# Performance work log

Measured on AMD Instinct MI355X. Metric: run time of the kernel, lower is better.

## Reference

```python
import jax, jax.numpy as jnp
import numpy as np

EPS = 1e-6
FRAME_SEQLEN = 1560          # hardcoded in source kv-cache path
LOCAL_ATTN_SIZE = 4
MAX_ATTN = LOCAL_ATTN_SIZE * FRAME_SEQLEN  # 6240
NUM_HEADS = 12


def _ln(x, w=None, b=None):
    mu = jnp.mean(x, axis=-1, keepdims=True)
    var = jnp.mean(jnp.square(x - mu), axis=-1, keepdims=True)
    y = (x - mu) * jax.lax.rsqrt(var + EPS)
    return y * w + b if w is not None else y


def _rms(x, w):
    return x * jax.lax.rsqrt(jnp.mean(jnp.square(x), axis=-1, keepdims=True) + EPS) * w


def _rope_tables(freqs_real, freqs_imag, nf, hh, ww, start_frame, c):
    # split freqs columns into temporal / height / width parts, as in causal_rope_apply
    s0 = c - 2 * (c // 3)
    s1 = c // 3
    def build(tab):
        f0 = tab[start_frame:start_frame + nf, :s0]       # [nf, s0]
        f1 = tab[:hh, s0:s0 + s1]                          # [hh, s1]
        f2 = tab[:ww, s0 + s1:]                            # [ww, s1]
        return jnp.concatenate([
            jnp.broadcast_to(f0[:, None, None, :], (nf, hh, ww, s0)),
            jnp.broadcast_to(f1[None, :, None, :], (nf, hh, ww, s1)),
            jnp.broadcast_to(f2[None, None, :, :], (nf, hh, ww, s1)),
        ], axis=-1).reshape(nf * hh * ww, 1, c)
    return build(freqs_real), build(freqs_imag)


def _causal_rope(x, cos, sin):
    # x: [B, L, n, d] with interleaved (real, imag) pairs; cos/sin: [1, L, 1, c]
    B, L, n, d = x.shape
    c = d // 2
    xr = x.reshape(B, L, n, c, 2)
    a, b = xr[..., 0], xr[..., 1]
    out = jnp.stack([a * cos - b * sin, a * sin + b * cos], axis=-1)
    return out.reshape(B, L, n, d)


def _sdpa(q, k, v):
    scale = q.shape[-1] ** -0.5
    s = jnp.einsum('bqhd,bkhd->bhqk', q, k) * scale
    a = jax.nn.softmax(s, axis=-1)
    return jnp.einsum('bhqk,bkhd->bqhd', a, v)


def _forward(hidden_states, encoder_hidden_states, temb, freqs_real, freqs_imag,
             k_cache, v_cache, scale_shift_table,
             Wq, bq, Wk, bk, Wv, bv, Wo, bo, norm_q_w, norm_k_w,
             saln_w, saln_b,
             cWq, cbq, cWk, cbk, cWv, cbv, cWo, cbo, c_norm_q_w, c_norm_k_w,
             W1, b1, W2, b2,
             current_start, grid_h, grid_w):
    B, L, D = hidden_states.shape
    nf = temb.shape[1]
    fs = L // nf                     # == FRAME_SEQLEN
    H = NUM_HEADS
    hd = D // H
    c = hd // 2
    x = hidden_states.astype(jnp.float32)

    # AdaLN modulation per frame
    e = scale_shift_table + temb                     # [B, nf, 6, D]
    shift, scale, gate = e[:, :, 0:1], e[:, :, 1:2], e[:, :, 2:3]
    c_shift, c_scale, c_gate = e[:, :, 3:4], e[:, :, 4:5], e[:, :, 5:6]

    nh = (_ln(x).reshape(B, nf, fs, D) * (1 + scale) + shift).reshape(B, L, D)

    # self-attn projections + rms_norm_across_heads qk norm
    q = _rms(nh @ Wq.T + bq, norm_q_w).reshape(B, L, H, hd)
    k = _rms(nh @ Wk.T + bk, norm_k_w).reshape(B, L, H, hd)
    v = (nh @ Wv.T + bv).reshape(B, L, H, hd)

    # causal RoPE with temporal offset current_start // 1560
    start_frame = current_start // FRAME_SEQLEN
    cos, sin = _rope_tables(freqs_real, freqs_imag, nf, grid_h, grid_w, start_frame, c)
    cos, sin = cos[None], sin[None]                  # [1, L, 1, c]
    rq = _causal_rope(q, cos, sin)
    rk = _causal_rope(k, cos, sin)

    # kv-cache update (no-eviction branch: num_new + local_end_prev == cache size)
    kc = jax.lax.stop_gradient(k_cache).at[:, current_start:current_start + L].set(rk)
    vc = jax.lax.stop_gradient(v_cache).at[:, current_start:current_start + L].set(v)
    local_end = current_start + L
    win_lo = max(0, local_end - MAX_ATTN)
    attn = _sdpa(rq, kc[:, win_lo:local_end], vc[:, win_lo:local_end]).reshape(B, L, D)
    attn = attn @ Wo.T + bo

    # gated residual + affine LN (self_attn_residual_norm)
    x = x + (attn.reshape(B, nf, fs, D) * gate).reshape(B, L, D)
    n2 = _ln(x, saln_w, saln_b)

    # T2V cross attention
    ctx = encoder_hidden_states.astype(jnp.float32)
    Lc = ctx.shape[1]
    cq = _rms(n2 @ cWq.T + cbq, c_norm_q_w).reshape(B, L, H, hd)
    ck = _rms(ctx @ cWk.T + cbk, c_norm_k_w).reshape(B, Lc, H, hd)
    cv = (ctx @ cWv.T + cbv).reshape(B, Lc, H, hd)
    ca = _sdpa(cq, ck, cv).reshape(B, L, D) @ cWo.T + cbo

    # residual + LN with c_scale/c_shift modulation (cross_attn_residual_norm)
    x = x + ca
    n3 = (_ln(x).reshape(B, nf, fs, D) * (1 + c_scale) + c_shift).reshape(B, L, D)

    # FFN (gelu tanh) + gated residual (MulAdd)
    ff = jax.nn.gelu(n3 @ W1.T + b1, approximate=True) @ W2.T + b2
    x = x + (ff.reshape(B, nf, fs, D) * c_gate).reshape(B, L, D)
    return x


def setup_inputs() -> dict:
    key = jax.random.key(0)
    D, FF, H = 1536, 8960, NUM_HEADS
    NF, FS = 2, FRAME_SEQLEN
    L = NF * FS
    CACHE = MAX_ATTN
    CTX = 512
    hd = D // H
    c = hd // 2
    ks = iter(jax.random.split(key, 40))
    def nrm(shape, s=1.0):
        return jax.random.normal(next(ks), shape, jnp.float32) * s

    def part(dim):
        inv = 1.0 / (10000.0 ** (np.arange(0, dim, 2, dtype=np.float64) / dim))
        f = np.outer(np.arange(1024, dtype=np.float64), inv)
        return np.cos(f), np.sin(f)
    c0, s0 = part(2 * (c - 2 * (c // 3)))
    c1, s1 = part(2 * (c // 3))
    c2, s2 = part(2 * (c // 3))
    freqs_real = jnp.asarray(np.concatenate([c0, c1, c2], axis=1), jnp.float32)  # [1024, 64]
    freqs_imag = jnp.asarray(np.concatenate([s0, s1, s2], axis=1), jnp.float32)

    return dict(
        hidden_states=nrm((1, L, D)),
        encoder_hidden_states=nrm((1, CTX, D)),
        temb=nrm((1, NF, 6, D), 0.5),
        freqs_real=freqs_real, freqs_imag=freqs_imag,
        k_cache=nrm((1, CACHE, H, hd), 0.5),
        v_cache=nrm((1, CACHE, H, hd), 0.5),
        scale_shift_table=nrm((1, 6, D), D ** -0.5),
        Wq=nrm((D, D), 0.02), bq=jnp.zeros((D,), jnp.float32),
        Wk=nrm((D, D), 0.02), bk=jnp.zeros((D,), jnp.float32),
        Wv=nrm((D, D), 0.02), bv=jnp.zeros((D,), jnp.float32),
        Wo=nrm((D, D), 0.02), bo=jnp.zeros((D,), jnp.float32),
        norm_q_w=jnp.ones((D,), jnp.float32), norm_k_w=jnp.ones((D,), jnp.float32),
        saln_w=jnp.ones((D,), jnp.float32), saln_b=jnp.zeros((D,), jnp.float32),
        cWq=nrm((D, D), 0.02), cbq=jnp.zeros((D,), jnp.float32),
        cWk=nrm((D, D), 0.02), cbk=jnp.zeros((D,), jnp.float32),
        cWv=nrm((D, D), 0.02), cbv=jnp.zeros((D,), jnp.float32),
        cWo=nrm((D, D), 0.02), cbo=jnp.zeros((D,), jnp.float32),
        c_norm_q_w=jnp.ones((D,), jnp.float32), c_norm_k_w=jnp.ones((D,), jnp.float32),
        W1=nrm((FF, D), 0.02), b1=jnp.zeros((FF,), jnp.float32),
        W2=nrm((D, FF), 0.02), b2=jnp.zeros((D,), jnp.float32),
        current_start=2 * FS, grid_h=30, grid_w=52,
    )


def reference(hidden_states, encoder_hidden_states, temb, freqs_real, freqs_imag,
              k_cache, v_cache, scale_shift_table,
              Wq, bq, Wk, bk, Wv, bv, Wo, bo, norm_q_w, norm_k_w,
              saln_w, saln_b,
              cWq, cbq, cWk, cbk, cWv, cbv, cWo, cbo, c_norm_q_w, c_norm_k_w,
              W1, b1, W2, b2,
              current_start, grid_h, grid_w):
    return _forward(hidden_states, encoder_hidden_states, temb, freqs_real, freqs_imag,
                    k_cache, v_cache, scale_shift_table,
                    Wq, bq, Wk, bk, Wv, bv, Wo, bo, norm_q_w, norm_k_w,
                    saln_w, saln_b,
                    cWq, cbq, cWk, cbk, cWv, cbv, cWo, cbo, c_norm_q_w, c_norm_k_w,
                    W1, b1, W2, b2,
                    current_start, grid_h, grid_w)
```

## Files before the change

### kernel.cpp

```cpp
#include <hip/hip_runtime.h>
#include <hip/hip_bf16.h>
#include <stdint.h>

typedef uint16_t u16;
typedef uint32_t u32;
typedef float    f32x4  __attribute__((ext_vector_type(4)));
typedef __bf16   bf16x8 __attribute__((ext_vector_type(8)));
typedef u16      u16x8  __attribute__((ext_vector_type(8)));
typedef u16      u16x4  __attribute__((ext_vector_type(4)));
typedef float    f32x4v __attribute__((ext_vector_type(4)));


__device__ __forceinline__ u16 f2bf(float f) {
    u32 u = __builtin_bit_cast(u32, f);
    u32 r = u + 0x7fffu + ((u >> 16) & 1u);
    return (u16)(r >> 16);
}
__device__ __forceinline__ float bfbits2f(u32 ubits) {
    return __builtin_bit_cast(float, ubits << 16);
}
__device__ __forceinline__ u32 cvtpk(float a, float b) {
    u32 r;
    asm("v_cvt_pk_bf16_f32 %0, %1, %2" : "=v"(r) : "v"(a), "v"(b));
    return r;
}
__device__ __forceinline__ bf16x8 loadb8(const u16* p) {
    u16x8 u = *(const u16x8*)p;
    return __builtin_bit_cast(bf16x8, u);
}
__device__ __forceinline__ f32x4 mfma16(bf16x8 a, bf16x8 b, f32x4 c) {
    return __builtin_amdgcn_mfma_f32_16x16x32_bf16(a, b, c, 0, 0, 0);
}
__device__ __forceinline__ void gload16(const u16* gp, u16* lp) {
    __builtin_amdgcn_global_load_lds((const __attribute__((address_space(1))) void*)gp,
                                     (__attribute__((address_space(3))) void*)lp, 16, 0, 0);
}
__device__ __forceinline__ float blockSum(float v, volatile float* buf, int t) {
#pragma unroll
    for (int o = 1; o < 64; o <<= 1) v += __shfl_xor(v, o);
    if ((t & 63) == 0) buf[t >> 6] = v;
    __syncthreads();
    float r = buf[0] + buf[1] + buf[2] + buf[3];
    __syncthreads();
    return r;
}

struct ConvJob { const float* s; u16* d; int n4; };
struct ConvJobs { ConvJob j[12]; int cnt; };

__global__ void k_conv(ConvJobs js) {
    int tid = blockIdx.x * blockDim.x + threadIdx.x;
    int stride = gridDim.x * blockDim.x;
    for (int q = 0; q < js.cnt; q++) {
        const f32x4v* s = (const f32x4v*)js.j[q].s;
        u16x4* d = (u16x4*)js.j[q].d;
        int n4 = js.j[q].n4;
        for (int i = tid; i < n4; i += stride) {
            f32x4v v = s[i];
            u16x4 o;
            o[0] = f2bf(v[0]); o[1] = f2bf(v[1]); o[2] = f2bf(v[2]); o[3] = f2bf(v[3]);
            d[i] = o;
        }
    }
}

__global__ void k_mod(const float* __restrict__ sst, const float* __restrict__ temb, float* __restrict__ e) {
    int i = blockIdx.x * 256 + threadIdx.x;
    if (i < 18432) e[i] = sst[i % 9216] + temb[i];
}

__global__ void k_cachecvt(const float* __restrict__ kc, const float* __restrict__ vc,
                           u16* __restrict__ Ka, u16* __restrict__ Va) {
    int b = blockIdx.x;
    int hd = (b % 6) * 256 + threadIdx.x;
    int p0 = (b / 6) * 4;
    int h = hd >> 7, d = hd & 127;
    u16x4 vv;
#pragma unroll
    for (int j = 0; j < 4; j++) {
        long src = (long)(p0 + j) * 1536 + hd;
        Ka[(long)h * 798720 + (long)(p0 + j) * 128 + d] = f2bf(kc[src]);
        vv[j] = f2bf(vc[src]);
    }
    *(u16x4*)&Va[(long)h * 798720 + (long)d * 6240 + p0] = vv;
}

__global__ __launch_bounds__(256) void k_ln(const float* __restrict__ x, u16* __restrict__ out,
                                            const float* __restrict__ mulp, const float* __restrict__ addp,
                                            int perFrame, int plusOne) {
    __shared__ float buf[4];
    const int row = blockIdx.x, t = threadIdx.x;
    const float* xr = x + (long)row * 1536;
    float v[6];
    float s = 0.f;
#pragma unroll
    for (int k = 0; k < 6; k++) { v[k] = xr[t + k * 256]; s += v[k]; }
    s = blockSum(s, buf, t);
    float mu = s * (1.f / 1536.f);
    float q = 0.f;
#pragma unroll
    for (int k = 0; k < 6; k++) { float d = v[k] - mu; q += d * d; }
    q = blockSum(q, buf, t);
    float inv = rsqrtf(q * (1.f / 1536.f) + 1e-6f);
    const int fo = perFrame ? (row / 1560) * 9216 : 0;
    u16* orow = out + (long)row * 1536;
    float add1 = plusOne ? 1.f : 0.f;
#pragma unroll
    for (int k = 0; k < 6; k++) {
        int c = t + k * 256;
        float m = mulp[fo + c] + add1;
        float y = (v[k] - mu) * inv * m + addp[fo + c];
        orow[c] = f2bf(y);
    }
}

__global__ __launch_bounds__(256) void k_rmsrope(const u16* __restrict__ in, int ld, int colOff,
                                                 const float* __restrict__ bias,
                                                 const float* __restrict__ w,
                                                 u16* __restrict__ out, long headStride,
                                                 const float* __restrict__ fr, const float* __restrict__ fi,
                                                 int doRope) {
    __shared__ float buf[4];
    const int row = blockIdx.x, t = threadIdx.x;
    const u32* xr = (const u32*)(in + (long)row * ld + colOff);
    const float2* b2 = (const float2*)bias;
    float px[3], py[3];
    float ss = 0.f;
#pragma unroll
    for (int i = 0; i < 3; i++) {
        u32 u = xr[t * 3 + i];
        float2 bb = b2[t * 3 + i];
        px[i] = bfbits2f(u & 0xffffu) + bb.x;
        py[i] = bfbits2f(u >> 16) + bb.y;
        ss += px[i] * px[i] + py[i] * py[i];
    }
    ss = blockSum(ss, buf, t);
    float inv = rsqrtf(ss * (1.f / 1536.f) + 1e-6f);
    int frame = 0, gh = 0, gw = 0;
    if (doRope) { frame = row / 1560; int rem = row - frame * 1560; gh = rem / 52; gw = rem - gh * 52; }
    const float2* w2 = (const float2*)w;
#pragma unroll
    for (int i = 0; i < 3; i++) {
        int jg = t * 3 + i;
        int hh = jg >> 6, j = jg & 63;
        float2 ww = w2[jg];
        float a = px[i] * inv * ww.x, b = py[i] * inv * ww.y;
        float oa = a, ob = b;
        if (doRope) {
            int fidx = (j < 22) ? (2 + frame) : ((j < 43) ? gh : gw);
            float cs = fr[fidx * 64 + j], sn = fi[fidx * 64 + j];
            oa = a * cs - b * sn;
            ob = a * sn + b * cs;
        }
        u16* dst = out + (long)hh * headStride + (long)row * 128 + j * 2;
        dst[0] = f2bf(oa);
        dst[1] = f2bf(ob);
    }
}

__global__ void k_scatterT(const u16* __restrict__ in, int ld, int colOff,
                           const float* __restrict__ bias, u16* __restrict__ outT,
                           int vstride, int posOff) {
    int hd = blockIdx.x * 256 + threadIdx.x;
    int r0 = blockIdx.y * 4;
    int h = hd >> 7, d = hd & 127;
    float bi = bias[hd];
    u16x4 pk;
#pragma unroll
    for (int j = 0; j < 4; j++)
        pk[j] = f2bf(bfbits2f(in[(long)(r0 + j) * ld + colOff + hd]) + bi);
    *(u16x4*)&outT[(long)h * 128 * vstride + (long)d * vstride + posOff + r0] = pk;
}

struct GemmP {
    const u16* A; const u16* B; void* C;
    const float* bias; const float* gate; const float* resid;
    int M, N, K, ldA, ldB, ldC, kChunk;
};

template <int EPI, int BM>
__global__ __launch_bounds__(256) void k_gemm(GemmP g) {
    constexpr int WM = BM / 2;
    constexpr int TM = BM / 32;
    __shared__ alignas(16) u16 As[BM * 32];
    __shared__ alignas(16) u16 Bs[128 * 32];
    const int t = threadIdx.x;
    const int w = t >> 6, l = t & 63, lr = l & 15, lg = l >> 4;
    const int wm = w >> 1, wn = w & 1;
    const long m0 = (long)blockIdx.y * BM, n0 = (long)blockIdx.x * 128;
    f32x4 acc[TM][4];
#pragma unroll
    for (int a = 0; a < TM; a++)
#pragma unroll
        for (int b = 0; b < 4; b++) acc[a][b] = f32x4{0.f, 0.f, 0.f, 0.f};

    const int rowU = t >> 2, c8 = t & 3;
    long arow[2], brow[2];
#pragma unroll
    for (int i = 0; i < 2; i++) {
        long r = m0 + rowU + i * 64;
        if (r > (long)g.M - 1) r = g.M - 1;
        arow[i] = r;
        brow[i] = n0 + rowU + i * 64;
    }

    const int kBeg = blockIdx.z * g.kChunk;
    const int kEnd = min(g.K, kBeg + g.kChunk);
    for (int k0 = kBeg; k0 < kEnd; k0 += 32) {
        __syncthreads();
#pragma unroll
        for (int i = 0; i < BM / 64; i++)
            gload16(g.A + arow[i] * (long)g.ldA + k0 + c8 * 8, &As[(i * 256 + w * 64) * 8]);
#pragma unroll
        for (int i = 0; i < 2; i++)
            gload16(g.B + brow[i] * (long)g.ldB + k0 + c8 * 8, &Bs[(i * 256 + w * 64) * 8]);
        __syncthreads();
        bf16x8 am[TM], bn[4];
#pragma unroll
        for (int mi = 0; mi < TM; mi++) am[mi] = loadb8(&As[(wm * WM + mi * 16 + lr) * 32 + lg * 8]);
#pragma unroll
        for (int ni = 0; ni < 4; ni++) bn[ni] = loadb8(&Bs[(wn * 64 + ni * 16 + lr) * 32 + lg * 8]);
#pragma unroll
        for (int mi = 0; mi < TM; mi++)
#pragma unroll
            for (int ni = 0; ni < 4; ni++)
                acc[mi][ni] = mfma16(am[mi], bn[ni], acc[mi][ni]);
    }

#pragma unroll
    for (int mi = 0; mi < TM; mi++) {
#pragma unroll
        for (int ni = 0; ni < 4; ni++) {
            long col = n0 + wn * 64 + ni * 16 + lr;
            float bi = g.bias ? g.bias[col] : 0.f;
#pragma unroll
            for (int r = 0; r < 4; r++) {
                long row = m0 + wm * WM + mi * 16 + lg * 4 + r;
                if (row >= g.M) continue;
                float v = acc[mi][ni][r] + bi;
                if constexpr (EPI == 0) {
                    ((float*)g.C)[row * g.ldC + col] = v;
                } else if constexpr (EPI == 1) {
                    ((u16*)g.C)[row * g.ldC + col] = f2bf(v);
                } else if constexpr (EPI == 2) {
                    float x3 = v * v * v;
                    float gl = 0.5f * v * (1.f + tanhf(0.79788456080286536f * (v + 0.044715f * x3)));
                    ((u16*)g.C)[row * g.ldC + col] = f2bf(gl);
                } else if constexpr (EPI == 3) {
                    float gt = g.gate ? g.gate[(row / 1560) * 9216 + col] : 1.f;
                    ((float*)g.C)[row * g.ldC + col] = g.resid[row * g.ldC + col] + v * gt;
                } else {
                    ((float*)g.C)[(long)blockIdx.z * ((long)g.M * g.ldC) + row * g.ldC + col] = v;
                }
            }
        }
    }
}

__global__ void k_gcomb(const float* __restrict__ P, int S, long MN4,
                        const float* __restrict__ bias, const float* __restrict__ gate,
                        const float* __restrict__ resid, float* __restrict__ out) {
    long i = (long)blockIdx.x * 256 + threadIdx.x;
    if (i >= MN4) return;
    f32x4v a = ((const f32x4v*)P)[i];
#pragma unroll 3
    for (int s = 1; s < S; s++) {
        f32x4v b = ((const f32x4v*)P)[(long)s * MN4 + i];
        a[0] += b[0]; a[1] += b[1]; a[2] += b[2]; a[3] += b[3];
    }
    long e0 = i * 4;
    int col = (int)(e0 % 1536);
    int fo = (int)((e0 / 1536) / 1560) * 9216;
    f32x4v r = ((const f32x4v*)resid)[i];
#pragma unroll
    for (int j = 0; j < 4; j++)
        r[j] += (a[j] + bias[col + j]) * gate[fo + col + j];
    ((f32x4v*)out)[i] = r;
}

__global__ void k_sumbf(const float* __restrict__ P, int S, long N4, u16* __restrict__ out) {
    long i = (long)blockIdx.x * 256 + threadIdx.x;
    if (i >= N4) return;
    f32x4v a = ((const f32x4v*)P)[i];
#pragma unroll 3
    for (int s = 1; s < S; s++) {
        f32x4v b = ((const f32x4v*)P)[(long)s * N4 + i];
        a[0] += b[0]; a[1] += b[1]; a[2] += b[2]; a[3] += b[3];
    }
    u16x4 o;
    o[0] = f2bf(a[0]); o[1] = f2bf(a[1]); o[2] = f2bf(a[2]); o[3] = f2bf(a[3]);
    ((u16x4*)out)[i] = o;
}

__global__ __launch_bounds__(256) void k_flash(const u16* __restrict__ Qb, const u16* __restrict__ Kb,
                                               const u16* __restrict__ Vtg,
                                               u16* __restrict__ Opart, float2* __restrict__ ms,
                                               int kvStride, int qlen, int splitIters, int totIters) {
    __shared__ alignas(16) u16 Pt[4][32 * 40];
    const int t = threadIdx.x;
    const int w = t >> 6, l = t & 63, lr = l & 15, lg = l >> 4;
    const int head = blockIdx.y, z = blockIdx.z;
    const long q0 = (long)blockIdx.x * 128;
    const u16* Qh = Qb + (long)head * qlen * 128;
    const u16* Kh = Kb + (long)head * (long)kvStride * 128;
    const u16* Vh = Vtg + (long)head * (long)kvStride * 128;
    constexpr float SCL2 = 0.08838834764831845f * 1.44269504088896f;

    bf16x8 aq[2][4];
#pragma unroll
    for (int wq = 0; wq < 2; wq++)
#pragma unroll
        for (int c = 0; c < 4; c++) {
            long row = q0 + w * 32 + wq * 16 + lr;
            if (row > (long)qlen - 1) row = qlen - 1;
            aq[wq][c] = loadb8(Qh + row * 128 + c * 32 + lg * 8);
        }

    f32x4 o[2][8];
    float mrow[2] = {-1e30f, -1e30f}, srow[2] = {0.f, 0.f};
#pragma unroll
    for (int wq = 0; wq < 2; wq++)
#pragma unroll
        for (int db = 0; db < 8; db++) o[wq][db] = f32x4{0.f, 0.f, 0.f, 0.f};

    const int it0 = z * splitIters;
    const int itN = min(totIters, it0 + splitIters);
    for (int kt = it0; kt < itN; kt++) {
        const long k0 = (long)kt * 32;

        f32x4 s[2][2];
        {
            bf16x8 kf[2][4];
#pragma unroll
            for (int kh = 0; kh < 2; kh++)
#pragma unroll
                for (int cb = 0; cb < 4; cb++)
                    kf[kh][cb] = loadb8(Kh + (k0 + kh * 16 + lr) * 128 + cb * 32 + lg * 8);
            __builtin_amdgcn_s_setprio(1);
#pragma unroll
            for (int kh = 0; kh < 2; kh++)
#pragma unroll
                for (int wq = 0; wq < 2; wq++) {
                    f32x4 acc = f32x4{0.f, 0.f, 0.f, 0.f};
#pragma unroll
                    for (int cb = 0; cb < 4; cb++) acc = mfma16(kf[kh][cb], aq[wq][cb], acc);
                    s[wq][kh] = acc;
                }
            __builtin_amdgcn_s_setprio(0);
        }

        bf16x8 vf[8];
#pragma unroll
        for (int db = 0; db < 8; db++)
            vf[db] = loadb8(Vh + (long)(db * 16 + lr) * kvStride + k0 + lg * 8);

#pragma unroll
        for (int wq = 0; wq < 2; wq++) {
            float pm = fmaxf(fmaxf(fmaxf(s[wq][0][0], s[wq][0][1]), fmaxf(s[wq][0][2], s[wq][0][3])),
                             fmaxf(fmaxf(s[wq][1][0], s[wq][1][1]), fmaxf(s[wq][1][2], s[wq][1][3])));
            pm = fmaxf(pm, __shfl_xor(pm, 16));
            pm = fmaxf(pm, __shfl_xor(pm, 32));
            float pm2 = pm * SCL2;
            if (__any(pm2 > mrow[wq] + 8.f)) {
                float nm = fmaxf(mrow[wq], pm2);
                float fsc = exp2f(mrow[wq] - nm);
                mrow[wq] = nm;
                srow[wq] *= fsc;
#pragma unroll
                for (int db = 0; db < 8; db++) {
                    f32x4 t4 = o[wq][db];
                    t4[0] *= fsc; t4[1] *= fsc; t4[2] *= fsc; t4[3] *= fsc;
                    o[wq][db] = t4;
                }
            }
            float p[8];
#pragma unroll
            for (int kh = 0; kh < 2; kh++)
#pragma unroll
                for (int r = 0; r < 4; r++)
                    p[kh * 4 + r] = exp2f(fmaf(s[wq][kh][r], SCL2, -mrow[wq]));
            float ts = ((p[0] + p[1]) + (p[2] + p[3])) + ((p[4] + p[5]) + (p[6] + p[7]));
            ts += __shfl_xor(ts, 16);
            ts += __shfl_xor(ts, 32);
            srow[wq] += ts;
            u32 w0 = cvtpk(p[0], p[1]), w1 = cvtpk(p[2], p[3]);
            u32 w2 = cvtpk(p[4], p[5]), w3 = cvtpk(p[6], p[7]);
            u16* pp = &Pt[w][(wq * 16 + lr) * 40 + lg * 4];
            *(u32*)pp = w0;
            *(u32*)(pp + 2) = w1;
            *(u32*)(pp + 16) = w2;
            *(u32*)(pp + 18) = w3;
        }

        bf16x8 pb0 = loadb8(&Pt[w][lr * 40 + lg * 8]);
        bf16x8 pb1 = loadb8(&Pt[w][(16 + lr) * 40 + lg * 8]);
        __builtin_amdgcn_s_setprio(1);
#pragma unroll
        for (int db = 0; db < 8; db++) {
            o[0][db] = mfma16(vf[db], pb0, o[0][db]);
            o[1][db] = mfma16(vf[db], pb1, o[1][db]);
        }
        __builtin_amdgcn_s_setprio(0);
    }

    const long part = ((long)z * 12 + head) * qlen;
#pragma unroll
    for (int wq = 0; wq < 2; wq++) {
        long row = q0 + w * 32 + wq * 16 + lr;
        if (row < qlen) {
            if (lg == 0) {
                float2 v; v.x = mrow[wq]; v.y = srow[wq];
                ms[part + row] = v;
            }
#pragma unroll
            for (int db = 0; db < 8; db++) {
                u16x4 pk;
#pragma unroll
                for (int r = 0; r < 4; r++) pk[r] = f2bf(o[wq][db][r]);
                *(u16x4*)&Opart[(part + row) * 128 + db * 16 + lg * 4] = pk;
            }
        }
    }
}

__global__ __launch_bounds__(256) void k_combine(const u16* __restrict__ Opart, const float2* __restrict__ ms,
                                                 u16* __restrict__ Ob, int qlen, int S) {
    int idx = blockIdx.x * 4 + (threadIdx.x >> 6);
    int l = threadIdx.x & 63;
    int h = idx / qlen, q = idx - h * qlen;
    float2 mm[6];
    float M = -1e30f;
    for (int s = 0; s < S; s++) {
        mm[s] = ms[((long)s * 12 + h) * qlen + q];
        M = fmaxf(M, mm[s].x);
    }
    float den = 0.f, a0 = 0.f, a1 = 0.f;
    for (int s = 0; s < S; s++) {
        float wgt = exp2f(mm[s].x - M);
        den += wgt * mm[s].y;
        u32 two = *(const u32*)&Opart[(((long)s * 12 + h) * qlen + q) * 128 + l * 2];
        a0 += wgt * bfbits2f(two & 0xffffu);
        a1 += wgt * bfbits2f(two >> 16);
    }
    float inv = 1.f / den;
    u32 o = ((u32)f2bf(a1 * inv) << 16) | (u32)f2bf(a0 * inv);
    *(u32*)&Ob[(long)q * 1536 + h * 128 + l * 2] = o;
}

extern "C" void kernel_launch(void* const* d_in, const int* in_sizes, int n_in,
                              void* d_out, int out_size, void* d_ws, size_t ws_size,
                              hipStream_t stream) {
    const float* hs    = (const float*)d_in[0];
    const float* ctx   = (const float*)d_in[1];
    const float* temb  = (const float*)d_in[2];
    const float* fr    = (const float*)d_in[3];
    const float* fi    = (const float*)d_in[4];
    const float* kcache= (const float*)d_in[5];
    const float* vcache= (const float*)d_in[6];
    const float* sst   = (const float*)d_in[7];
    const float* Wq = (const float*)d_in[8],  *bq = (const float*)d_in[9];
    const float* Wk = (const float*)d_in[10], *bk = (const float*)d_in[11];
    const float* Wv = (const float*)d_in[12], *bv = (const float*)d_in[13];
    const float* Wo = (const float*)d_in[14], *bo = (const float*)d_in[15];
    const float* nqw = (const float*)d_in[16], *nkw = (const float*)d_in[17];
    const float* salnw = (const float*)d_in[18], *salnb = (const float*)d_in[19];
    const float* cWq = (const float*)d_in[20], *cbq = (const float*)d_in[21];
    const float* cWk = (const float*)d_in[22], *cbk = (const float*)d_in[23];
    const float* cWv = (const float*)d_in[24], *cbv = (const float*)d_in[25];
    const float* cWo = (const float*)d_in[26], *cbo = (const float*)d_in[27];
    const float* cnqw = (const float*)d_in[28], *cnkw = (const float*)d_in[29];
    const float* W1 = (const float*)d_in[30], *b1 = (const float*)d_in[31];
    const float* W2 = (const float*)d_in[32], *b2 = (const float*)d_in[33];
    float* out = (float*)d_out;

    char* base = (char*)d_ws;
    size_t off = 0;
    auto alloc = [&](size_t bytes) -> char* {
        char* p = base + off;
        off = (off + bytes + 255) & ~(size_t)255;
        return p;
    };
    float* e   = (float*)alloc(18432 * 4);
    u16* nbuf  = (u16*)alloc((size_t)3120 * 1536 * 2);
    u16* lin   = (u16*)alloc((size_t)3120 * 4608 * 2);
    u16* Qb    = (u16*)alloc((size_t)12 * 3120 * 128 * 2);
    u16* Ka    = (u16*)alloc((size_t)12 * 6240 * 128 * 2);
    u16* Va    = (u16*)alloc((size_t)12 * 6240 * 128 * 2);
    u16* attnb = (u16*)alloc((size_t)3120 * 1536 * 2);
    float* X1  = (float*)alloc((size_t)3120 * 1536 * 4);
    u16* CKb   = (u16*)alloc((size_t)12 * 512 * 128 * 2);
    u16* CVt   = (u16*)alloc((size_t)12 * 512 * 128 * 2);
    u16* H1    = (u16*)alloc((size_t)3120 * 8960 * 2);
    u16* wqkv_b= (u16*)alloc((size_t)4608 * 1536 * 2);
    u16* wo_b  = (u16*)alloc((size_t)1536 * 1536 * 2);
    u16* cwq_b = (u16*)alloc((size_t)1536 * 1536 * 2);
    u16* cwkv_b= (u16*)alloc((size_t)3072 * 1536 * 2);
    u16* cwo_b = (u16*)alloc((size_t)1536 * 1536 * 2);
    u16* w1_b  = (u16*)alloc((size_t)8960 * 1536 * 2);
    u16* w2_b  = (u16*)alloc((size_t)8960 * 1536 * 2);
    u16* ctxb  = (u16*)alloc((size_t)512 * 1536 * 2);

    u16* Opart = H1;
    float2* msb = (float2*)lin;
    float* pbuf = (float*)lin;
    float* cpart = (float*)H1;

    ConvJobs cj{};
    auto setj = [&](int i, const float* s, u16* d, int n) { cj.j[i].s = s; cj.j[i].d = d; cj.j[i].n4 = n / 4; };
    setj(0, Wq, wqkv_b, 1536 * 1536);
    setj(1, Wk, wqkv_b + (size_t)1536 * 1536, 1536 * 1536);
    setj(2, Wv, wqkv_b + (size_t)2 * 1536 * 1536, 1536 * 1536);
    setj(3, Wo, wo_b, 1536 * 1536);
    setj(4, cWq, cwq_b, 1536 * 1536);
    setj(5, cWk, cwkv_b, 1536 * 1536);
    setj(6, cWv, cwkv_b + (size_t)1536 * 1536, 1536 * 1536);
    setj(7, cWo, cwo_b, 1536 * 1536);
    setj(8, W1, w1_b, 8960 * 1536);
    setj(9, W2, w2_b, 8960 * 1536);
    setj(10, ctx, ctxb, 512 * 1536);
    cj.cnt = 11;
    k_conv<<<2048, 256, 0, stream>>>(cj);

    k_mod<<<72, 256, 0, stream>>>(sst, temb, e);
    k_cachecvt<<<4680, 256, 0, stream>>>(kcache, vcache, Ka, Va);

    k_ln<<<3120, 256, 0, stream>>>(hs, nbuf, e + 1536, e + 0, 1, 1);

    GemmP gqkv{nbuf, wqkv_b, lin, nullptr, nullptr, nullptr, 3120, 4608, 1536, 1536, 1536, 4608, 1536};
    k_gemm<1, 128><<<dim3(36, 25), 256, 0, stream>>>(gqkv);
    k_rmsrope<<<3120, 256, 0, stream>>>(lin, 4608, 0, bq, nqw, Qb, (long)3120 * 128, fr, fi, 1);
    k_rmsrope<<<3120, 256, 0, stream>>>(lin, 4608, 1536, bk, nkw, Ka + (size_t)3120 * 128, (long)6240 * 128, fr, fi, 1);
    k_scatterT<<<dim3(6, 780), 256, 0, stream>>>(lin, 4608, 3072, bv, Va, 6240, 3120);

    k_flash<<<dim3(25, 12, 5), 256, 0, stream>>>(Qb, Ka, Va, Opart, msb, 6240, 3120, 39, 195);
    k_combine<<<9360, 256, 0, stream>>>(Opart, msb, attnb, 3120, 5);

    GemmP gwo{attnb, wo_b, X1, bo, e + 2 * 1536, hs, 3120, 1536, 1536, 1536, 1536, 1536, 1536};
    k_gemm<3, 64><<<dim3(12, 49), 256, 0, stream>>>(gwo);

    k_ln<<<3120, 256, 0, stream>>>(X1, nbuf, salnw, salnb, 0, 0);

    GemmP gcq{nbuf, cwq_b, lin, nullptr, nullptr, nullptr, 3120, 1536, 1536, 1536, 1536, 1536, 1536};
    k_gemm<1, 64><<<dim3(12, 49), 256, 0, stream>>>(gcq);
    k_rmsrope<<<3120, 256, 0, stream>>>(lin, 1536, 0, cbq, cnqw, Qb, (long)3120 * 128, fr, fi, 0);

    GemmP gckv{ctxb, cwkv_b, cpart, nullptr, nullptr, nullptr, 512, 3072, 1536, 1536, 1536, 3072, 384};
    k_gemm<5, 64><<<dim3(24, 8, 4), 256, 0, stream>>>(gckv);
    k_sumbf<<<1536, 256, 0, stream>>>(cpart, 4, 393216, lin);
    k_rmsrope<<<512, 256, 0, stream>>>(lin, 3072, 0, cbk, cnkw, CKb, (long)512 * 128, fr, fi, 0);
    k_scatterT<<<dim3(6, 128), 256, 0, stream>>>(lin, 3072, 1536, cbv, CVt, 512, 0);

    k_flash<<<dim3(25, 12, 4), 256, 0, stream>>>(Qb, CKb, CVt, Opart, msb, 512, 3120, 4, 16);
    k_combine<<<9360, 256, 0, stream>>>(Opart, msb, attnb, 3120, 4);

    GemmP gcwo{attnb, cwo_b, X1, cbo, nullptr, X1, 3120, 1536, 1536, 1536, 1536, 1536, 1536};
    k_gemm<3, 64><<<dim3(12, 49), 256, 0, stream>>>(gcwo);

    k_ln<<<3120, 256, 0, stream>>>(X1, nbuf, e + 4 * 1536, e + 3 * 1536, 1, 1);

    GemmP g1{nbuf, w1_b, H1, b1, nullptr, nullptr, 3120, 8960, 1536, 1536, 1536, 8960, 1536};
    k_gemm<2, 128><<<dim3(70, 25), 256, 0, stream>>>(g1);

    GemmP g2{H1, w2_b, pbuf, nullptr, nullptr, nullptr, 3120, 1536, 8960, 8960, 8960, 1536, 2240};
    k_gemm<5, 128><<<dim3(12, 25, 4), 256, 0, stream>>>(g2);
    k_gcomb<<<4680, 256, 0, stream>>>(pbuf, 4, 1198080, b2, e + 5 * 1536, X1, out);
}
```

Before: 1.212 ms.

## Stage K and V tiles in shared memory for flash attention

Each iteration now loads the 32-key K tile and the transposed V tile cooperatively into LDS with two barriers, instead of every wave reading them separately from global memory. Waves then read their MFMA fragments from LDS. The intent is to cut redundant global and L2 traffic, since four waves previously each fetched the same K/V. The cost is two __syncthreads per iteration with no double buffering, extra LDS, and the removal of the setprio hints. It also renames the stride parameter to kvLen, which assumes the caller's stride equals the KV length.

```diff
diff --git a/kernel.cpp b/kernel.cpp
--- a/kernel.cpp
+++ b/kernel.cpp
@@ -295,15 +295,17 @@
 __global__ __launch_bounds__(256) void k_flash(const u16* __restrict__ Qb, const u16* __restrict__ Kb,
                                                const u16* __restrict__ Vtg,
                                                u16* __restrict__ Opart, float2* __restrict__ ms,
-                                               int kvStride, int qlen, int splitIters, int totIters) {
+                                               int kvLen, int qlen, int splitIters, int totIters) {
+    __shared__ alignas(16) u16 Kt[32 * 136];
+    __shared__ alignas(16) u16 Vt[128 * 40];
     __shared__ alignas(16) u16 Pt[4][32 * 40];
     const int t = threadIdx.x;
     const int w = t >> 6, l = t & 63, lr = l & 15, lg = l >> 4;
     const int head = blockIdx.y, z = blockIdx.z;
     const long q0 = (long)blockIdx.x * 128;
     const u16* Qh = Qb + (long)head * qlen * 128;
-    const u16* Kh = Kb + (long)head * (long)kvStride * 128;
-    const u16* Vh = Vtg + (long)head * (long)kvStride * 128;
+    const u16* Kh = Kb + (long)head * kvLen * 128;
+    const u16* Vh = Vtg + (long)head * kvLen * 128;
     constexpr float SCL2 = 0.08838834764831845f * 1.44269504088896f;
 
     bf16x8 aq[2][4];
@@ -323,36 +325,41 @@
 #pragma unroll
         for (int db = 0; db < 8; db++) o[wq][db] = f32x4{0.f, 0.f, 0.f, 0.f};
 
+    const int kr = t >> 4, c16 = (t & 15) * 8;
+    const int vr = t >> 1, vh = (t & 1) * 16;
+
     const int it0 = z * splitIters;
     const int itN = min(totIters, it0 + splitIters);
     for (int kt = it0; kt < itN; kt++) {
         const long k0 = (long)kt * 32;
+        __syncthreads();
+        {
+            u16x8 a0 = *(const u16x8*)(Kh + (k0 + kr) * 128 + c16);
+            u16x8 a1 = *(const u16x8*)(Kh + (k0 + kr + 16) * 128 + c16);
+            *(u16x8*)&Kt[kr * 136 + c16] = a0;
+            *(u16x8*)&Kt[(kr + 16) * 136 + c16] = a1;
+            u16x8 b0 = *(const u16x8*)(Vh + (long)vr * kvLen + k0 + vh);
+            u16x8 b1 = *(const u16x8*)(Vh + (long)vr * kvLen + k0 + vh + 8);
+            *(u16x8*)&Vt[vr * 40 + vh] = b0;
+            *(u16x8*)&Vt[vr * 40 + vh + 8] = b1;
+        }
+        __syncthreads();
 
         f32x4 s[2][2];
-        {
-            bf16x8 kf[2][4];
-#pragma unroll
-            for (int kh = 0; kh < 2; kh++)
-#pragma unroll
-                for (int cb = 0; cb < 4; cb++)
-                    kf[kh][cb] = loadb8(Kh + (k0 + kh * 16 + lr) * 128 + cb * 32 + lg * 8);
-            __builtin_amdgcn_s_setprio(1);
-#pragma unroll
-            for (int kh = 0; kh < 2; kh++)
-#pragma unroll
-                for (int wq = 0; wq < 2; wq++) {
-                    f32x4 acc = f32x4{0.f, 0.f, 0.f, 0.f};
-#pragma unroll
-                    for (int cb = 0; cb < 4; cb++) acc = mfma16(kf[kh][cb], aq[wq][cb], acc);
-                    s[wq][kh] = acc;
-                }
-            __builtin_amdgcn_s_setprio(0);
-        }
-
-        bf16x8 vf[8];
-#pragma unroll
-        for (int db = 0; db < 8; db++)
-            vf[db] = loadb8(Vh + (long)(db * 16 + lr) * kvStride + k0 + lg * 8);
+#pragma unroll
+        for (int kh = 0; kh < 2; kh++) {
+            bf16x8 kf[4];
+#pragma unroll
+            for (int cb = 0; cb < 4; cb++)
+                kf[cb] = loadb8(&Kt[(kh * 16 + lr) * 136 + cb * 32 + lg * 8]);
+#pragma unroll
+            for (int wq = 0; wq < 2; wq++) {
+                f32x4 acc = f32x4{0.f, 0.f, 0.f, 0.f};
+#pragma unroll
+                for (int cb = 0; cb < 4; cb++) acc = mfma16(kf[cb], aq[wq][cb], acc);
+                s[wq][kh] = acc;
+            }
+        }
 
 #pragma unroll
         for (int wq = 0; wq < 2; wq++) {
@@ -394,13 +401,12 @@
 
         bf16x8 pb0 = loadb8(&Pt[w][lr * 40 + lg * 8]);
         bf16x8 pb1 = loadb8(&Pt[w][(16 + lr) * 40 + lg * 8]);
-        __builtin_amdgcn_s_setprio(1);
 #pragma unroll
         for (int db = 0; db < 8; db++) {
-            o[0][db] = mfma16(vf[db], pb0, o[0][db]);
-            o[1][db] = mfma16(vf[db], pb1, o[1][db]);
-        }
-        __builtin_amdgcn_s_setprio(0);
+            bf16x8 vf = loadb8(&Vt[(db * 16 + lr) * 40 + lg * 8]);
+            o[0][db] = mfma16(vf, pb0, o[0][db]);
+            o[1][db] = mfma16(vf, pb1, o[1][db]);
+        }
     }
 
     const long part = ((long)z * 12 + head) * qlen;
```

Result: faster. 1.095 ms (-9.7%).
